# Kernel tuning notes

Measured on AMD Instinct MI355X. Metric: run time of the kernel, lower is better.

Reference implementation:

```python
import jax, jax.numpy as jnp
import numpy as np

N = 100_000   # nodes per type
E = 800_000   # edges per relation
H = 128       # hidden_channels
O = 64        # out_channels
TIME_SCALE = 1.0
LN_EPS = 1e-5


def setup_inputs() -> dict:
    key = jax.random.key(0)
    ks = jax.random.split(key, 24)
    nrm = lambda k, shp, s=1.0: jax.random.normal(k, shp, jnp.float32) * s
    inp = {}
    inp["x_A"] = nrm(ks[0], (N, H))
    inp["x_B"] = nrm(ks[1], (N, H))
    inp["x_C"] = nrm(ks[2], (N, H))
    inp["t_A"] = jax.random.uniform(ks[3], (N,), jnp.float32) * 1000.0
    inp["t_B"] = jax.random.uniform(ks[4], (N,), jnp.float32) * 1000.0
    inp["t_C"] = jax.random.uniform(ks[5], (N,), jnp.float32) * 1000.0
    inp["edge1"] = jnp.stack([jax.random.randint(ks[6], (E,), 0, N),
                              jax.random.randint(ks[7], (E,), 0, N)]).astype(jnp.int32)
    inp["edge2"] = jnp.stack([jax.random.randint(ks[8], (E,), 0, N),
                              jax.random.randint(ks[9], (E,), 0, N)]).astype(jnp.int32)
    kk = 10
    for i in range(2):
        inp[f"Wl{i}"] = nrm(ks[kk], (H, H), 0.05); kk += 1
        inp[f"bl{i}"] = jnp.zeros((H,), jnp.float32)
        inp[f"W0{i}"] = nrm(ks[kk], (H, H), 0.05); kk += 1
        inp[f"b0{i}"] = jnp.zeros((H,), jnp.float32)
        inp[f"W1{i}"] = nrm(ks[kk], (H, H), 0.05); kk += 1
        inp[f"b1{i}"] = jnp.zeros((H,), jnp.float32)
        inp[f"gate{i}"] = jnp.asarray(0.5, jnp.float32)
        inp[f"lam{i}"] = jnp.asarray(0.1, jnp.float32)  # raw lambda
        inp[f"lng{i}"] = jnp.ones((H,), jnp.float32)
        inp[f"lnb{i}"] = jnp.zeros((H,), jnp.float32)
    inp["Wout"] = nrm(ks[kk], (H, O), 0.05)
    inp["bout"] = jnp.zeros((O,), jnp.float32)
    return inp


def _layer(h_src, h_dst, x0_dst, edge, t_src, t_dst,
           Wl, bl, W0, b0, W1, b1, gate, raw_lam, lng, lnb):
    s, d = edge[0], edge[1]
    n_dst = h_dst.shape[0]
    # per-edge time-decay weight
    lam = jax.nn.softplus(raw_lam) + 1e-8
    delta = jnp.maximum((t_dst[d] - t_src[s]) / TIME_SCALE, 0.0)
    w = jnp.exp(jnp.maximum(-lam * delta, -60.0))          # [E]
    # gather + weight + scatter-add  (propagate with aggr='add')
    msg = h_src[s] * w[:, None]                            # [E,H]
    agg = jax.ops.segment_sum(msg, d, num_segments=n_dst)  # [n_dst,H]
    deg = jnp.maximum(jax.ops.segment_sum(w, d, num_segments=n_dst), 1e-6)
    out = agg / deg[:, None]
    g = jax.nn.sigmoid(gate)
    y = out @ Wl + bl + (1.0 - g) * (h_dst @ W0 + b0) + g * (x0_dst @ W1 + b1)
    y = jax.nn.relu(y)
    mu = jnp.mean(y, axis=-1, keepdims=True)
    var = jnp.mean((y - mu) ** 2, axis=-1, keepdims=True)
    y = (y - mu) * jax.lax.rsqrt(var + LN_EPS) * lng + lnb
    # index_copy_: only nodes that appear as a destination get updated
    cnt = jax.ops.segment_sum(jnp.ones_like(w), d, num_segments=n_dst)
    return jnp.where((cnt > 0)[:, None], y, h_dst)


def reference(x_A, x_B, x_C, t_A, t_B, t_C, edge1, edge2,
              Wl0, bl0, W00, b00, W10, b10, gate0, lam0, lng0, lnb0,
              Wl1, bl1, W01, b01, W11, b11, gate1, lam1, lng1, lnb1,
              Wout, bout):
    # reversed(metapath): process (B,r2,C) with conv_idx=1 first, then (A,r1,B) with conv_idx=0
    h_C = _layer(x_B, x_C, x_C, edge2, t_B, t_C,
                 Wl1, bl1, W01, b01, W11, b11, gate1, lam1, lng1, lnb1)
    h_B = _layer(x_A, x_B, x_B, edge1, t_A, t_B,
                 Wl0, bl0, W00, b00, W10, b10, gate0, lam0, lng0, lnb0)
    del h_B  # target type is metapath[-1][2] == 'C'; B's update does not feed C
    return h_C @ Wout + bout
```

## Files before the change

### kernel.cpp

```cpp
#include <hip/hip_runtime.h>


#define HD 128
#define OD 64
#define SCAN_E 1024

typedef unsigned short u16;
typedef short v8s __attribute__((ext_vector_type(8)));
typedef float v4f __attribute__((ext_vector_type(4)));

union Frag {
    unsigned int u[4];
    uint4 q;
    v8s v;
};

__device__ __forceinline__ float softplus_f(float x) {
    return fmaxf(x, 0.0f) + log1pf(expf(-fabsf(x)));
}
__device__ __forceinline__ float sigmoid_f(float x) {
    return 1.0f / (1.0f + expf(-x));
}
__device__ __forceinline__ int swz(int r, int c) {
    int g = (c >> 2) ^ (r & 7);
    return r * 128 + g * 4 + (c & 3);
}

__device__ __forceinline__ void split_store(float x, u16* ph, u16* pl) {
    unsigned int b = __float_as_uint(x);
    unsigned int h = b & 0xffff0000u;
    *ph = (u16)(h >> 16);
    float r = x - __uint_as_float(h);
    *pl = (u16)(__float_as_uint(r) >> 16);
}

__device__ __forceinline__ void cvt_split8(const float* f, unsigned int* hi,
                                           unsigned int* lo) {
#pragma unroll
    for (int j = 0; j < 4; ++j) {
        unsigned int b0 = __float_as_uint(f[2 * j]);
        unsigned int b1 = __float_as_uint(f[2 * j + 1]);
        unsigned int h0 = b0 & 0xffff0000u;
        unsigned int h1 = b1 & 0xffff0000u;
        hi[j] = (h0 >> 16) | h1;
        float r0 = f[2 * j]     - __uint_as_float(h0);
        float r1 = f[2 * j + 1] - __uint_as_float(h1);
        lo[j] = (__float_as_uint(r0) >> 16) | (__float_as_uint(r1) & 0xffff0000u);
    }
}

__global__ __launch_bounds__(256) void k_hist(
    const int* __restrict__ edge, int* __restrict__ cnt, int E)
{
    int e = blockIdx.x * 256 + threadIdx.x;
    if (e < E) atomicAdd(cnt + edge[E + e], 1);
}

__global__ __launch_bounds__(256) void k_scan1(
    const int* __restrict__ cnt, int* __restrict__ offs,
    int* __restrict__ part, int N)
{
    __shared__ int sh[256];
    const int t = threadIdx.x;
    const int base = blockIdx.x * SCAN_E + t * 4;
    int v[4], sum = 0;
#pragma unroll
    for (int i = 0; i < 4; ++i) {
        int idx = base + i;
        v[i] = (idx < N) ? cnt[idx] : 0;
        sum += v[i];
    }
    sh[t] = sum;
    __syncthreads();
    for (int off = 1; off < 256; off <<= 1) {
        int x = (t >= off) ? sh[t - off] : 0;
        __syncthreads();
        sh[t] += x;
        __syncthreads();
    }
    int run = (t > 0) ? sh[t - 1] : 0;
    if (t == 255) part[blockIdx.x] = sh[t];
#pragma unroll
    for (int i = 0; i < 4; ++i) {
        int idx = base + i;
        if (idx < N) offs[idx] = run;
        run += v[i];
    }
}

__global__ __launch_bounds__(128) void k_scan2(int* __restrict__ part, int NB)
{
    __shared__ int sh[128];
    const int t = threadIdx.x;
    sh[t] = (t < NB) ? part[t] : 0;
    __syncthreads();
    for (int off = 1; off < 128; off <<= 1) {
        int x = (t >= off) ? sh[t - off] : 0;
        __syncthreads();
        sh[t] += x;
        __syncthreads();
    }
    if (t < NB) part[t] = (t > 0) ? sh[t - 1] : 0;
}

__global__ __launch_bounds__(256) void k_fillw(
    const int* __restrict__ edge, const float* __restrict__ tB,
    const float* __restrict__ tC, const float* __restrict__ lam_raw,
    const int* __restrict__ offs, const int* __restrict__ part,
    int* __restrict__ fillc, int2* __restrict__ srcw, int E)
{
    int e = blockIdx.x * 256 + threadIdx.x;
    if (e >= E) return;
    int s = edge[e];
    int d = edge[E + e];
    float lam = softplus_f(lam_raw[0]) + 1e-8f;
    float dt  = fmaxf(tC[d] - tB[s], 0.0f);
    float w   = expf(fmaxf(-lam * dt, -60.0f));
    int pos = offs[d] + part[d >> 10] + atomicAdd(fillc + d, 1);
    srcw[pos] = make_int2(s, __float_as_int(w));
}

__global__ __launch_bounds__(256) void k_wprep(
    const float* __restrict__ Wl, const float* __restrict__ W0,
    const float* __restrict__ W1, const float* __restrict__ Wout,
    const float* __restrict__ bl, const float* __restrict__ b0,
    const float* __restrict__ b1, const float* __restrict__ gatep,
    u16* __restrict__ wlh, u16* __restrict__ wll,
    u16* __restrict__ wch, u16* __restrict__ wcl,
    u16* __restrict__ woh, u16* __restrict__ wol, float* __restrict__ bc)
{
    int i = blockIdx.x * 256 + threadIdx.x;
    const float g = sigmoid_f(gatep[0]);
    if (i < 16384) {
        int n = i >> 7, k = i & 127;
        float a  = Wl[k * 128 + n];
        float w0 = W0[k * 128 + n];
        float w1 = W1[k * 128 + n];
        float c  = (1.f - g) * w0 + g * w1;
        int off = ((k >> 5) * 128 + n) * 32 + (k & 31);
        split_store(a, wlh + off, wll + off);
        split_store(c, wch + off, wcl + off);
    } else if (i < 24576) {
        int j = i - 16384;
        int n = j >> 7, k = j & 127;
        float v = Wout[k * 64 + n];
        int off = ((k >> 5) * 64 + n) * 32 + (k & 31);
        split_store(v, woh + off, wol + off);
    } else if (i < 24704) {
        int t = i - 24576;
        bc[t] = bl[t] + (1.f - g) * b0[t] + g * b1[t];
    }
}

__global__ __launch_bounds__(256) void k_gather(
    const float* __restrict__ xB, const int2* __restrict__ srcw,
    const int* __restrict__ offs, const int* __restrict__ part,
    const int* __restrict__ cnt, float* __restrict__ aggn, int N)
{
    const int wave = (blockIdx.x * 256 + threadIdx.x) >> 6;
    const int lane = threadIdx.x & 63;
    const int slot = lane >> 4;
    const int l4   = lane & 15;
    if (wave >= N) return;
    const int r    = wave;
    const int degc = cnt[r];

    float* dstp = aggn + (size_t)r * HD;
    if (degc == 0) {
        if (slot == 0) {
            *reinterpret_cast<float4*>(dstp + l4 * 4) = make_float4(0, 0, 0, 0);
            *reinterpret_cast<float4*>(dstp + 64 + l4 * 4) = make_float4(0, 0, 0, 0);
        }
        return;
    }

    const int start = offs[r] + part[r >> 10];
    float4 a0 = make_float4(0, 0, 0, 0), a1 = make_float4(0, 0, 0, 0);
    float sw = 0.f;
    for (int j = slot; j < degc; j += 4) {
        int2 swp = srcw[start + j];
        float w = __int_as_float(swp.y);
        const float* row = xB + (size_t)swp.x * HD;
        float4 x0 = *reinterpret_cast<const float4*>(row + l4 * 4);
        float4 x1 = *reinterpret_cast<const float4*>(row + 64 + l4 * 4);
        a0.x = fmaf(w, x0.x, a0.x); a0.y = fmaf(w, x0.y, a0.y);
        a0.z = fmaf(w, x0.z, a0.z); a0.w = fmaf(w, x0.w, a0.w);
        a1.x = fmaf(w, x1.x, a1.x); a1.y = fmaf(w, x1.y, a1.y);
        a1.z = fmaf(w, x1.z, a1.z); a1.w = fmaf(w, x1.w, a1.w);
        sw += w;
    }
#pragma unroll
    for (int m = 16; m <= 32; m <<= 1) {
        a0.x += __shfl_xor(a0.x, m); a0.y += __shfl_xor(a0.y, m);
        a0.z += __shfl_xor(a0.z, m); a0.w += __shfl_xor(a0.w, m);
        a1.x += __shfl_xor(a1.x, m); a1.y += __shfl_xor(a1.y, m);
        a1.z += __shfl_xor(a1.z, m); a1.w += __shfl_xor(a1.w, m);
        sw   += __shfl_xor(sw, m);
    }
    float inv = 1.0f / fmaxf(sw, 1e-6f);
    if (slot == 0) {
        a0.x *= inv; a0.y *= inv; a0.z *= inv; a0.w *= inv;
        a1.x *= inv; a1.y *= inv; a1.z *= inv; a1.w *= inv;
        *reinterpret_cast<float4*>(dstp + l4 * 4) = a0;
        *reinterpret_cast<float4*>(dstp + 64 + l4 * 4) = a1;
    }
}

__global__ __launch_bounds__(256) void k_fused(
    const float* __restrict__ xC, const float* __restrict__ aggn,
    const int* __restrict__ cnt,
    const u16* __restrict__ wlh, const u16* __restrict__ wll,
    const u16* __restrict__ wch, const u16* __restrict__ wcl,
    const u16* __restrict__ woh, const u16* __restrict__ wol,
    const float* __restrict__ bc, const float* __restrict__ lng,
    const float* __restrict__ lnb, const float* __restrict__ bout,
    float* __restrict__ out, int N)
{
    __shared__ float lds[4 * 32 * 128];

    const int lane = threadIdx.x & 63;
    const int wid  = threadIdx.x >> 6;
    const int lr   = lane & 15;
    const int kb   = lane >> 4;
    const int row0 = blockIdx.x * 128 + wid * 32;
    float* myl = lds + wid * 32 * 128;

    v4f acc[2][8] = {};

#pragma unroll
    for (int mat = 0; mat < 2; ++mat) {
        const float* Asrc = mat ? xC : aggn;
        const uint4* BH = (const uint4*)(mat ? wch : wlh);
        const uint4* BL = (const uint4*)(mat ? wcl : wll);
#pragma unroll
        for (int kc = 0; kc < 4; ++kc) {
            Frag ah[2], al[2];
#pragma unroll
            for (int rt = 0; rt < 2; ++rt) {
                int r = row0 + rt * 16 + lr;
                r = (r < N) ? r : (N - 1);
                const float4* ap = (const float4*)(
                    Asrc + (size_t)r * HD + kc * 32 + kb * 8);
                float4 u0 = ap[0], u1 = ap[1];
                float f[8] = {u0.x, u0.y, u0.z, u0.w, u1.x, u1.y, u1.z, u1.w};
                cvt_split8(f, ah[rt].u, al[rt].u);
            }
#pragma unroll
            for (int ct = 0; ct < 8; ++ct) {
                int idx = kc * 512 + (ct * 16 + lr) * 4 + kb;
                Frag bh, bl;
                bh.q = BH[idx];
                bl.q = BL[idx];
#pragma unroll
                for (int rt = 0; rt < 2; ++rt) {
                    acc[rt][ct] = __builtin_amdgcn_mfma_f32_16x16x32_bf16(
                        ah[rt].v, bh.v, acc[rt][ct], 0, 0, 0);
                    acc[rt][ct] = __builtin_amdgcn_mfma_f32_16x16x32_bf16(
                        ah[rt].v, bl.v, acc[rt][ct], 0, 0, 0);
                    acc[rt][ct] = __builtin_amdgcn_mfma_f32_16x16x32_bf16(
                        al[rt].v, bh.v, acc[rt][ct], 0, 0, 0);
                }
            }
        }
    }

    float bcv[8], gav[8], bev[8];
#pragma unroll
    for (int ct = 0; ct < 8; ++ct) {
        int c = ct * 16 + lr;
        bcv[ct] = bc[c];
        gav[ct] = lng[c];
        bev[ct] = lnb[c];
    }

#pragma unroll
    for (int rt = 0; rt < 2; ++rt) {
        int rq = row0 + rt * 16 + kb * 4;
        int cvr[4] = {0, 0, 0, 0};
        if (rq < N) {
            int4 cv = *(const int4*)(cnt + rq);
            cvr[0] = cv.x; cvr[1] = cv.y; cvr[2] = cv.z; cvr[3] = cv.w;
        }
#pragma unroll
        for (int reg = 0; reg < 4; ++reg) {
            int rloc = rt * 16 + kb * 4 + reg;
            int r    = rq + reg;
            float yv[8];
            float s = 0.f, q = 0.f;
#pragma unroll
            for (int ct = 0; ct < 8; ++ct) {
                float v = acc[rt][ct][reg] + bcv[ct];
                v = fmaxf(v, 0.0f);
                yv[ct] = v;
                s += v;
                q += v * v;
            }
#pragma unroll
            for (int m = 1; m < 16; m <<= 1) {
                s += __shfl_xor(s, m);
                q += __shfl_xor(q, m);
            }
            float mu   = s * (1.0f / 128.0f);
            float var  = q * (1.0f / 128.0f) - mu * mu;
            float rstd = rsqrtf(var + 1e-5f);

            if (r < N) {
                if (cvr[reg] > 0) {
#pragma unroll
                    for (int ct = 0; ct < 8; ++ct)
                        myl[swz(rloc, ct * 16 + lr)] =
                            (yv[ct] - mu) * rstd * gav[ct] + bev[ct];
                } else {
                    size_t base = (size_t)r * HD;
#pragma unroll
                    for (int ct = 0; ct < 8; ++ct)
                        myl[swz(rloc, ct * 16 + lr)] = xC[base + ct * 16 + lr];
                }
            } else {
#pragma unroll
                for (int ct = 0; ct < 8; ++ct)
                    myl[swz(rloc, ct * 16 + lr)] = 0.0f;
            }
        }
    }

    __syncthreads();

    v4f acc2[2][4] = {};
    const uint4* BH = (const uint4*)woh;
    const uint4* BL = (const uint4*)wol;

#pragma unroll
    for (int kc = 0; kc < 4; ++kc) {
        Frag ah[2], al[2];
#pragma unroll
        for (int rt = 0; rt < 2; ++rt) {
            int rloc = rt * 16 + lr;
            int c0   = kc * 32 + kb * 8;
            float4 u0 = *reinterpret_cast<const float4*>(&myl[swz(rloc, c0)]);
            float4 u1 = *reinterpret_cast<const float4*>(&myl[swz(rloc, c0 + 4)]);
            float f[8] = {u0.x, u0.y, u0.z, u0.w, u1.x, u1.y, u1.z, u1.w};
            cvt_split8(f, ah[rt].u, al[rt].u);
        }
#pragma unroll
        for (int ct = 0; ct < 4; ++ct) {
            int idx = kc * 256 + (ct * 16 + lr) * 4 + kb;
            Frag bh, bl;
            bh.q = BH[idx];
            bl.q = BL[idx];
#pragma unroll
            for (int rt = 0; rt < 2; ++rt) {
                acc2[rt][ct] = __builtin_amdgcn_mfma_f32_16x16x32_bf16(
                    ah[rt].v, bh.v, acc2[rt][ct], 0, 0, 0);
                acc2[rt][ct] = __builtin_amdgcn_mfma_f32_16x16x32_bf16(
                    ah[rt].v, bl.v, acc2[rt][ct], 0, 0, 0);
                acc2[rt][ct] = __builtin_amdgcn_mfma_f32_16x16x32_bf16(
                    al[rt].v, bh.v, acc2[rt][ct], 0, 0, 0);
            }
        }
    }

    float bov[4];
#pragma unroll
    for (int ct = 0; ct < 4; ++ct) bov[ct] = bout[ct * 16 + lr];

#pragma unroll
    for (int rt = 0; rt < 2; ++rt) {
#pragma unroll
        for (int reg = 0; reg < 4; ++reg) {
            int r = row0 + rt * 16 + kb * 4 + reg;
            if (r < N) {
#pragma unroll
                for (int ct = 0; ct < 4; ++ct)
                    out[(size_t)r * OD + ct * 16 + lr] =
                        acc2[rt][ct][reg] + bov[ct];
            }
        }
    }
}

extern "C" void kernel_launch(void* const* d_in, const int* in_sizes, int n_in,
                              void* d_out, int out_size, void* d_ws, size_t ws_size,
                              hipStream_t stream) {
    const float* xB    = (const float*)d_in[1];
    const float* xC    = (const float*)d_in[2];
    const float* tB    = (const float*)d_in[4];
    const float* tC    = (const float*)d_in[5];
    const int*   edge2 = (const int*)d_in[7];
    const float* Wl1   = (const float*)d_in[18];
    const float* bl1   = (const float*)d_in[19];
    const float* W01   = (const float*)d_in[20];
    const float* b01   = (const float*)d_in[21];
    const float* W11   = (const float*)d_in[22];
    const float* b11   = (const float*)d_in[23];
    const float* gate1 = (const float*)d_in[24];
    const float* lam1  = (const float*)d_in[25];
    const float* lng1  = (const float*)d_in[26];
    const float* lnb1  = (const float*)d_in[27];
    const float* Wout  = (const float*)d_in[28];
    const float* bout  = (const float*)d_in[29];

    const int N = in_sizes[2] / HD;
    const int E = in_sizes[7] / 2;

    int*   cnt   = (int*)d_ws;
    int*   fillc = cnt + N;
    int*   offs  = fillc + N;
    int*   part  = offs + N;
    int2*  srcw  = (int2*)(part + 128);
    u16*   wlh   = (u16*)(srcw + E);
    u16*   wll   = wlh + 16384;
    u16*   wch   = wll + 16384;
    u16*   wcl   = wch + 16384;
    u16*   woh   = wcl + 16384;
    u16*   wol   = woh + 8192;
    float* bc    = (float*)(wol + 8192);
    float* buf   = bc + 128;

    hipMemsetAsync(cnt, 0, (size_t)2 * N * sizeof(int), stream);

    dim3 blk(256);
    const int gE = (E + 255) / 256;
    const int NB = (N + SCAN_E - 1) / SCAN_E;

    k_wprep<<<97, blk, 0, stream>>>(Wl1, W01, W11, Wout, bl1, b01, b11, gate1,
                                    wlh, wll, wch, wcl, woh, wol, bc);
    k_hist <<<gE, blk, 0, stream>>>(edge2, cnt, E);
    k_scan1<<<NB, blk, 0, stream>>>(cnt, offs, part, N);
    k_scan2<<<1, 128, 0, stream>>>(part, NB);
    k_fillw<<<gE, blk, 0, stream>>>(edge2, tB, tC, lam1, offs, part, fillc, srcw, E);

    const int gN64 = (N * 64 + 255) / 256;
    k_gather<<<gN64, blk, 0, stream>>>(xB, srcw, offs, part, cnt, buf, N);

    const int GB = (N + 127) / 128;
    k_fused<<<GB, blk, 0, stream>>>(xC, buf, cnt, wlh, wll, wch, wcl, woh, wol,
                                    bc, lng1, lnb1, bout, (float*)d_out, N);
}
```

Baseline: 220.4 us.

## Run output GEMM per 16-row tile to halve LDS and drop the block barrier

The fused kernel now finishes the LayerNorm result for one 16-row tile, then immediately runs the output projection on it before moving to the next tile. This halves the per-wave LDS staging buffer and the output accumulator registers, and drops the block-wide __syncthreads, since each wave only reads back its own LDS region. The goal is higher occupancy and less synchronization, at the cost of a serialized per-tile schedule. The edge-gather loop in the aggregation kernel is also unrolled by two to keep more loads in flight.

```diff
diff --git a/kernel.cpp b/kernel.cpp
--- a/kernel.cpp
+++ b/kernel.cpp
@@ -177,6 +177,7 @@
     const int start = offs[r] + part[r >> 10];
     float4 a0 = make_float4(0, 0, 0, 0), a1 = make_float4(0, 0, 0, 0);
     float sw = 0.f;
+#pragma unroll 2
     for (int j = slot; j < degc; j += 4) {
         int2 swp = srcw[start + j];
         float w = __int_as_float(swp.y);
@@ -216,14 +217,14 @@
     const float* __restrict__ lnb, const float* __restrict__ bout,
     float* __restrict__ out, int N)
 {
-    __shared__ float lds[4 * 32 * 128];
+    __shared__ float lds[4 * 16 * 128];
 
     const int lane = threadIdx.x & 63;
     const int wid  = threadIdx.x >> 6;
     const int lr   = lane & 15;
     const int kb   = lane >> 4;
     const int row0 = blockIdx.x * 128 + wid * 32;
-    float* myl = lds + wid * 32 * 128;
+    float* myl = lds + wid * 16 * 128;
 
     v4f acc[2][8] = {};
 
@@ -272,6 +273,12 @@
         gav[ct] = lng[c];
         bev[ct] = lnb[c];
     }
+    float bov[4];
+#pragma unroll
+    for (int ct = 0; ct < 4; ++ct) bov[ct] = bout[ct * 16 + lr];
+
+    const uint4* BH3 = (const uint4*)woh;
+    const uint4* BL3 = (const uint4*)wol;
 
 #pragma unroll
     for (int rt = 0; rt < 2; ++rt) {
@@ -283,7 +290,7 @@
         }
 #pragma unroll
         for (int reg = 0; reg < 4; ++reg) {
-            int rloc = rt * 16 + kb * 4 + reg;
+            int rloc = kb * 4 + reg;
             int r    = rq + reg;
             float yv[8];
             float s = 0.f, q = 0.f;
@@ -322,58 +329,40 @@
                     myl[swz(rloc, ct * 16 + lr)] = 0.0f;
             }
         }
-    }
-
-    __syncthreads();
-
-    v4f acc2[2][4] = {};
-    const uint4* BH = (const uint4*)woh;
-    const uint4* BL = (const uint4*)wol;
-
-#pragma unroll
-    for (int kc = 0; kc < 4; ++kc) {
-        Frag ah[2], al[2];
-#pragma unroll
-        for (int rt = 0; rt < 2; ++rt) {
-            int rloc = rt * 16 + lr;
-            int c0   = kc * 32 + kb * 8;
-            float4 u0 = *reinterpret_cast<const float4*>(&myl[swz(rloc, c0)]);
-            float4 u1 = *reinterpret_cast<const float4*>(&myl[swz(rloc, c0 + 4)]);
-            float f[8] = {u0.x, u0.y, u0.z, u0.w, u1.x, u1.y, u1.z, u1.w};
-            cvt_split8(f, ah[rt].u, al[rt].u);
-        }
-#pragma unroll
-        for (int ct = 0; ct < 4; ++ct) {
-            int idx = kc * 256 + (ct * 16 + lr) * 4 + kb;
-            Frag bh, bl;
-            bh.q = BH[idx];
-            bl.q = BL[idx];
-#pragma unroll
-            for (int rt = 0; rt < 2; ++rt) {
-                acc2[rt][ct] = __builtin_amdgcn_mfma_f32_16x16x32_bf16(
-                    ah[rt].v, bh.v, acc2[rt][ct], 0, 0, 0);
-                acc2[rt][ct] = __builtin_amdgcn_mfma_f32_16x16x32_bf16(
-                    ah[rt].v, bl.v, acc2[rt][ct], 0, 0, 0);
-                acc2[rt][ct] = __builtin_amdgcn_mfma_f32_16x16x32_bf16(
-                    al[rt].v, bh.v, acc2[rt][ct], 0, 0, 0);
-            }
-        }
-    }
-
-    float bov[4];
-#pragma unroll
-    for (int ct = 0; ct < 4; ++ct) bov[ct] = bout[ct * 16 + lr];
-
-#pragma unroll
-    for (int rt = 0; rt < 2; ++rt) {
+
+        v4f acc2[4] = {};
+#pragma unroll
+        for (int kc = 0; kc < 4; ++kc) {
+            Frag ah, al;
+            {
+                int c0 = kc * 32 + kb * 8;
+                float4 u0 = *reinterpret_cast<const float4*>(&myl[swz(lr, c0)]);
+                float4 u1 = *reinterpret_cast<const float4*>(&myl[swz(lr, c0 + 4)]);
+                float f[8] = {u0.x, u0.y, u0.z, u0.w, u1.x, u1.y, u1.z, u1.w};
+                cvt_split8(f, ah.u, al.u);
+            }
+#pragma unroll
+            for (int ct = 0; ct < 4; ++ct) {
+                int idx = kc * 256 + (ct * 16 + lr) * 4 + kb;
+                Frag bh, bl;
+                bh.q = BH3[idx];
+                bl.q = BL3[idx];
+                acc2[ct] = __builtin_amdgcn_mfma_f32_16x16x32_bf16(
+                    ah.v, bh.v, acc2[ct], 0, 0, 0);
+                acc2[ct] = __builtin_amdgcn_mfma_f32_16x16x32_bf16(
+                    ah.v, bl.v, acc2[ct], 0, 0, 0);
+                acc2[ct] = __builtin_amdgcn_mfma_f32_16x16x32_bf16(
+                    al.v, bh.v, acc2[ct], 0, 0, 0);
+            }
+        }
+
 #pragma unroll
         for (int reg = 0; reg < 4; ++reg) {
-            int r = row0 + rt * 16 + kb * 4 + reg;
+            int r = rq + reg;
             if (r < N) {
 #pragma unroll
                 for (int ct = 0; ct < 4; ++ct)
-                    out[(size_t)r * OD + ct * 16 + lr] =
-                        acc2[rt][ct][reg] + bov[ct];
+                    out[(size_t)r * OD + ct * 16 + lr] = acc2[ct][reg] + bov[ct];
             }
         }
     }
```

Result: no change. 223.0 us (+1.1%).
